# Kernel tuning notes

Measured on AMD Instinct MI355X. Metric: run time of the kernel, lower is better.

## Reference

```python
import jax, jax.numpy as jnp
import numpy as np

D_MODEL = 1024
N_HEADS = 16
D_HEAD = D_MODEL // N_HEADS
SCALE = 1.0 / np.sqrt(D_HEAD).astype(np.float32)


def _feature_map(x):
    # phi(x) = elu(x) + 1
    return jax.nn.elu(x) + 1.0


def setup_inputs() -> dict:
    key = jax.random.key(0)
    ks = jax.random.split(key, 7)
    b, s = 4, 2048
    w = 1.0 / np.sqrt(D_MODEL).astype(np.float32)
    return {
        "x": jax.random.normal(ks[0], (b, s, D_MODEL), dtype=jnp.float32),
        "Wq": jax.random.normal(ks[1], (D_MODEL, D_MODEL), dtype=jnp.float32) * w,
        "Wk": jax.random.normal(ks[2], (D_MODEL, D_MODEL), dtype=jnp.float32) * w,
        "Wv": jax.random.normal(ks[3], (D_MODEL, D_MODEL), dtype=jnp.float32) * w,
        "Wo": jax.random.normal(ks[4], (D_MODEL, D_MODEL), dtype=jnp.float32) * w,
        "Wg": jax.random.normal(ks[5], (N_HEADS, D_MODEL), dtype=jnp.float32) * w,
        "bg": jax.random.normal(ks[6], (N_HEADS,), dtype=jnp.float32) * 0.02,
    }


def reference(x, Wq, Wk, Wv, Wo, Wg, bg):
    b, s, _ = x.shape
    # projections (PyTorch Linear: y = x @ W.T)
    q = (x @ Wq.T).reshape(b, s, N_HEADS, D_HEAD)
    k = (x @ Wk.T).reshape(b, s, N_HEADS, D_HEAD)
    v = (x @ Wv.T).reshape(b, s, N_HEADS, D_HEAD)
    q = _feature_map(q * SCALE)
    k = _feature_map(k)
    gate = jax.nn.sigmoid(x @ Wg.T + bg)  # [b, s, h]

    # time-major for scan: [s, b, h, dh] and [s, b, h]
    qt = jnp.moveaxis(q, 1, 0)
    kt = jnp.moveaxis(k, 1, 0)
    vt = jnp.moveaxis(v, 1, 0)
    gt = jnp.moveaxis(gate, 1, 0)

    S0 = jnp.zeros((b, N_HEADS, D_HEAD, D_HEAD), dtype=x.dtype)

    def step(S, inp):
        q_t, k_t, v_t, g_t = inp
        # S_t = g_t * S_{t-1} + k_t v_t^T
        S = g_t[:, :, None, None] * S + k_t[..., :, None] * v_t[..., None, :]
        y_t = jnp.einsum("bhi,bhij->bhj", q_t, S)
        return S, y_t

    _, ys = jax.lax.scan(step, S0, (qt, kt, vt, gt))  # ys: [s, b, h, dh]
    y = jnp.moveaxis(ys, 0, 1).reshape(b, s, D_MODEL)
    return y @ Wo.T
```

## Files before the change

### kernel.cpp

```cpp
#include <hip/hip_runtime.h>
#include <hip/hip_bf16.h>
#include <math.h>

#define BATCH 4
#define SEQ 2048
#define DMODEL 1024
#define NHEADS 16
#define DHEAD 64
#define MTOK (BATCH * SEQ)
#define SCALE_Q 0.125f
#define NCHAIN (BATCH * NHEADS)
#define CT 64
#define NC (SEQ / CT)
#define SP 72
#define QKVS 3072
#define WROWS 4224

typedef unsigned short ushort_t;
typedef __attribute__((ext_vector_type(8))) short bf16x8;
typedef __attribute__((ext_vector_type(4))) float f32x4;

__device__ __forceinline__ float bf2f(unsigned short u) {
    return __uint_as_float(((unsigned)u) << 16);
}
__device__ __forceinline__ unsigned short f2bf(float f) {
    unsigned u = __float_as_uint(f);
    return (unsigned short)((u + 0x7fffu + ((u >> 16) & 1u)) >> 16);
}

__global__ __launch_bounds__(256) void cvt_all(const float* __restrict__ x,
                                               const float* __restrict__ Wq,
                                               const float* __restrict__ Wk,
                                               const float* __restrict__ Wv,
                                               const float* __restrict__ Wo,
                                               const float* __restrict__ Wg,
                                               ushort_t* __restrict__ xb,
                                               ushort_t* __restrict__ wcat) {
    const int blk = blockIdx.x;
    const int tid = threadIdx.x;

    if (blk < MTOK) {
        const float* xr = x + (size_t)blk * DMODEL;
        float4 v = ((const float4*)xr)[tid];
        ushort4 o;
        o.x = f2bf(v.x); o.y = f2bf(v.y); o.z = f2bf(v.z); o.w = f2bf(v.w);
        ((ushort4*)(xb + (size_t)blk * DMODEL))[tid] = o;
    } else {
        const int row = blk - MTOK;
        ushort4 o;
        if (row >= 3088 && row < 3200) {
            o.x = o.y = o.z = o.w = 0;
        } else {
            const float* src;
            if (row < 1024)      src = Wq + (size_t)row * DMODEL;
            else if (row < 2048) src = Wk + (size_t)(row - 1024) * DMODEL;
            else if (row < 3072) src = Wv + (size_t)(row - 2048) * DMODEL;
            else if (row < 3088) src = Wg + (size_t)(row - 3072) * DMODEL;
            else                 src = Wo + (size_t)(row - 3200) * DMODEL;
            float4 v = ((const float4*)src)[tid];
            o.x = f2bf(v.x); o.y = f2bf(v.y); o.z = f2bf(v.z); o.w = f2bf(v.w);
        }
        ((ushort4*)(wcat + (size_t)row * DMODEL))[tid] = o;
    }
}

#define GT 128
#define GBK 32

__global__ __launch_bounds__(256) void gemm_bf16(const ushort_t* __restrict__ A,
                                                 const ushort_t* __restrict__ B,
                                                 float* __restrict__ Cf,
                                                 ushort_t* __restrict__ Cb,
                                                 float* __restrict__ gatep,
                                                 const float* __restrict__ bgp,
                                                 int M, int N, int K,
                                                 int mode) {
    __shared__ ushort_t As[2][GT * GBK];
    __shared__ ushort_t Bs[2][GT * GBK];

    const int tid = threadIdx.x;
    const int w = tid >> 6;
    const int l = tid & 63;

    const int flat = blockIdx.x;
    const int kx = flat & 7;
    const int ii = flat >> 3;
    const int bx = ii >> 3;
    const int by = (kx << 3) | (ii & 7);
    const int m0 = by * GT;
    const int n0 = bx * GT;

    const int wm = (w >> 1) * 64;
    const int wn = (w & 1) * 64;

    const int srow = l >> 2;
    const int schunk = ((l & 3) ^ ((l >> 3) & 3)) * 8;

    const ushort_t* aseg[2];
    const ushort_t* bseg[2];
#pragma unroll
    for (int i = 0; i < 2; ++i) {
        const int s = w * 2 + i;
        aseg[i] = A + (size_t)(m0 + s * 16 + srow) * K + schunk;
        bseg[i] = B + (size_t)(n0 + s * 16 + srow) * K + schunk;
    }

#define STAGE(buf, k0)                                                          \
    do {                                                                        \
        _Pragma("unroll")                                                       \
        for (int i_ = 0; i_ < 2; ++i_) {                                        \
            const int s_ = w * 2 + i_;                                          \
            __builtin_amdgcn_global_load_lds(                                   \
                (const __attribute__((address_space(1))) unsigned int*)(const void*)(aseg[i_] + (k0)), \
                (__attribute__((address_space(3))) unsigned int*)(void*)&As[buf][s_ * 16 * GBK], \
                16, 0, 0);                                                      \
            __builtin_amdgcn_global_load_lds(                                   \
                (const __attribute__((address_space(1))) unsigned int*)(const void*)(bseg[i_] + (k0)), \
                (__attribute__((address_space(3))) unsigned int*)(void*)&Bs[buf][s_ * 16 * GBK], \
                16, 0, 0);                                                      \
        }                                                                       \
    } while (0)

    f32x4 acc[4][4];
#pragma unroll
    for (int i = 0; i < 4; ++i)
#pragma unroll
        for (int j = 0; j < 4; ++j)
#pragma unroll
            for (int r = 0; r < 4; ++r) acc[i][j][r] = 0.f;

    const int fr = l & 15;
    const int fsw = (((l >> 4) ^ ((fr >> 1) & 3))) * 8;

    STAGE(0, 0);

    const int nit = K / GBK;
    for (int it = 0; it < nit; ++it) {
        __syncthreads();
        if (it + 1 < nit) STAGE((it + 1) & 1, (it + 1) * GBK);

        const ushort_t* __restrict__ as = As[it & 1];
        const ushort_t* __restrict__ bs = Bs[it & 1];

        bf16x8 af[4], bfr[4];
#pragma unroll
        for (int ti = 0; ti < 4; ++ti)
            af[ti] = *(const bf16x8*)&as[(wm + ti * 16 + fr) * GBK + fsw];
#pragma unroll
        for (int tj = 0; tj < 4; ++tj)
            bfr[tj] = *(const bf16x8*)&bs[(wn + tj * 16 + fr) * GBK + fsw];
#pragma unroll
        for (int ti = 0; ti < 4; ++ti)
#pragma unroll
            for (int tj = 0; tj < 4; ++tj)
                acc[ti][tj] = __builtin_amdgcn_mfma_f32_16x16x32_bf16(
                    af[ti], bfr[tj], acc[ti][tj], 0, 0, 0);
    }
#undef STAGE

    const int er = (l >> 4) * 4;
    const int ec = l & 15;

    if (mode == 3 && n0 == 3072) {
#pragma unroll
        for (int ti = 0; ti < 4; ++ti)
#pragma unroll
            for (int r = 0; r < 4; ++r) {
                if (wn == 0) {
                    const int row = m0 + wm + ti * 16 + er + r;
                    const float vv = acc[ti][0][r] + bgp[ec];
                    gatep[(size_t)row * NHEADS + ec] = 1.f / (1.f + __expf(-vv));
                }
            }
        return;
    }

    float escale = 1.0f;
    bool do_phi = false;
    if (mode == 3) {
        do_phi = (n0 < 2048);
        escale = (n0 < 1024) ? SCALE_Q : 1.0f;
    }

#pragma unroll
    for (int ti = 0; ti < 4; ++ti)
#pragma unroll
        for (int tj = 0; tj < 4; ++tj)
#pragma unroll
            for (int r = 0; r < 4; ++r) {
                const int row = m0 + wm + ti * 16 + er + r;
                const int col = n0 + wn + tj * 16 + ec;
                float val = acc[ti][tj][r];
                if (mode == 0) {
                    Cf[(size_t)row * N + col] = val;
                } else {
                    val *= escale;
                    if (do_phi) val = (val > 0.f) ? (val + 1.f) : __expf(val);
                    Cb[(size_t)row * QKVS + col] = f2bf(val);
                }
            }
}

__global__ __launch_bounds__(256) void p1_kernel(const ushort_t* __restrict__ qkv,
                                                 const float* __restrict__ gate,
                                                 float* __restrict__ Dt,
                                                 float* __restrict__ Bg) {
    const int tile = blockIdx.x;
    const int chain = tile >> 5;
    const int c = tile & 31;
    const int b = chain >> 4;
    const int h = chain & 15;
    const int tid = threadIdx.x;
    const int w = tid >> 6;
    const int l = tid & 63;

    __shared__ ushort_t Kt[DHEAD * SP];
    __shared__ ushort_t Vt[DHEAD * SP];
    __shared__ float bs[CT];

    const int tau = tid >> 2;
    const int seg = (tid & 3) * 16;
    const size_t grow = ((size_t)(b * SEQ + c * CT + tau)) * QKVS + h * DHEAD + seg;
    union { float4 f4[2]; ushort_t us[16]; } uk, uv;
    uk.f4[0] = *(const float4*)&qkv[grow + 1024];
    uk.f4[1] = *(const float4*)&qkv[grow + 1024 + 8];
    uv.f4[0] = *(const float4*)&qkv[grow + 2048];
    uv.f4[1] = *(const float4*)&qkv[grow + 2048 + 8];

    if (tid < 64) {
        float g = gate[((size_t)(b * SEQ + c * CT + tid)) * NHEADS + h];
        float lg = __logf(g);
#pragma unroll
        for (int d = 1; d < 64; d <<= 1) {
            float n = __shfl_up(lg, d, 64);
            if (l >= d) lg += n;
        }
        bs[tid] = lg;
        if (tid == 63) Bg[tile] = lg;
    }
    __syncthreads();

    const float e = __expf(bs[63] - bs[tau]);
#pragma unroll
    for (int f = 0; f < 16; ++f) {
        Kt[(seg + f) * SP + tau] = f2bf(e * bf2f(uk.us[f]));
        Vt[(seg + f) * SP + tau] = uv.us[f];
    }
    __syncthreads();

    const int fr = l & 15;
    const int fq = (l >> 4) * 8;
    const int jw = w * 16;

    f32x4 accD[4];
#pragma unroll
    for (int nt = 0; nt < 4; ++nt)
#pragma unroll
        for (int r = 0; r < 4; ++r) accD[nt][r] = 0.f;

#pragma unroll
    for (int kc = 0; kc < 2; ++kc) {
        bf16x8 va = *(const bf16x8*)&Vt[(jw + fr) * SP + kc * 32 + fq];
#pragma unroll
        for (int nt = 0; nt < 4; ++nt) {
            bf16x8 kf = *(const bf16x8*)&Kt[(nt * 16 + fr) * SP + kc * 32 + fq];
            accD[nt] = __builtin_amdgcn_mfma_f32_16x16x32_bf16(va, kf, accD[nt], 0, 0, 0);
        }
    }

    const int er = (l >> 4) * 4;
    const size_t dbase = (size_t)tile * (DHEAD * DHEAD);
#pragma unroll
    for (int nt = 0; nt < 4; ++nt)
#pragma unroll
        for (int r = 0; r < 4; ++r) {
            const int j = jw + er + r;
            const int i = nt * 16 + fr;
            Dt[dbase + j * DHEAD + i] = accD[nt][r];
        }
}

__global__ __launch_bounds__(256) void p2_kernel(const float* __restrict__ Dt,
                                                 const float* __restrict__ Bg,
                                                 ushort_t* __restrict__ St) {
    const int chain = blockIdx.x >> 2;
    const int jq = (blockIdx.x & 3) * 16;
    const int tid = threadIdx.x;
    const int jj = jq + (tid >> 4);
    const int ii = (tid & 15) * 4;

    float4 S = make_float4(0.f, 0.f, 0.f, 0.f);
    for (int c = 0; c < NC; ++c) {
        const size_t base = (((size_t)chain * NC + c) * DHEAD + jj) * DHEAD + ii;
        ushort4 o;
        o.x = f2bf(S.x); o.y = f2bf(S.y); o.z = f2bf(S.z); o.w = f2bf(S.w);
        *(ushort4*)&St[base] = o;
        const float eB = __expf(Bg[chain * NC + c]);
        const float4 D = *(const float4*)&Dt[base];
        S.x = eB * S.x + D.x;
        S.y = eB * S.y + D.y;
        S.z = eB * S.z + D.z;
        S.w = eB * S.w + D.w;
    }
}

__global__ __launch_bounds__(256) void p3_kernel(const ushort_t* __restrict__ qkv,
                                                 const ushort_t* __restrict__ St,
                                                 const float* __restrict__ gate,
                                                 ushort_t* __restrict__ yb) {
    const int tile = blockIdx.x;
    const int chain = tile >> 5;
    const int c = tile & 31;
    const int b = chain >> 4;
    const int h = chain & 15;
    const int tid = threadIdx.x;
    const int w = tid >> 6;
    const int l = tid & 63;

    __shared__ ushort_t Qs[CT * SP];
    __shared__ ushort_t Ks[CT * SP];
    __shared__ ushort_t Vt[DHEAD * SP];
    __shared__ ushort_t Ss[CT * SP];
    __shared__ ushort_t Ps[CT * SP];
    __shared__ float bs[CT];

    {
        const int row = tid >> 2;
        const int seg = (tid & 3) * 16;
        const size_t grow = ((size_t)(b * SEQ + c * CT + row)) * QKVS + h * DHEAD + seg;
        float4 q0 = *(const float4*)&qkv[grow];
        float4 q1 = *(const float4*)&qkv[grow + 8];
        float4 k0 = *(const float4*)&qkv[grow + 1024];
        float4 k1 = *(const float4*)&qkv[grow + 1024 + 8];
        union { float4 f4[2]; ushort_t us[16]; } uv;
        uv.f4[0] = *(const float4*)&qkv[grow + 2048];
        uv.f4[1] = *(const float4*)&qkv[grow + 2048 + 8];
        const size_t srow = (((size_t)chain * NC + c) * DHEAD + row) * DHEAD + seg;
        float4 s0 = *(const float4*)&St[srow];
        float4 s1 = *(const float4*)&St[srow + 8];
        *(float4*)&Qs[row * SP + seg]     = q0;
        *(float4*)&Qs[row * SP + seg + 8] = q1;
        *(float4*)&Ks[row * SP + seg]     = k0;
        *(float4*)&Ks[row * SP + seg + 8] = k1;
        *(float4*)&Ss[row * SP + seg]     = s0;
        *(float4*)&Ss[row * SP + seg + 8] = s1;
#pragma unroll
        for (int f = 0; f < 16; ++f)
            Vt[(seg + f) * SP + row] = uv.us[f];
    }
    if (tid < 64) {
        float g = gate[((size_t)(b * SEQ + c * CT + tid)) * NHEADS + h];
        float lg = __logf(g);
#pragma unroll
        for (int d = 1; d < 64; d <<= 1) {
            float n = __shfl_up(lg, d, 64);
            if (l >= d) lg += n;
        }
        bs[tid] = lg;
    }
    __syncthreads();

    const int fr = l & 15;
    const int fq = (l >> 4) * 8;
    const int tw = w * 16;

    bf16x8 qa[2];
#pragma unroll
    for (int kc = 0; kc < 2; ++kc)
        qa[kc] = *(const bf16x8*)&Qs[(tw + fr) * SP + kc * 32 + fq];

    f32x4 accA[4], accP[4];
#pragma unroll
    for (int nt = 0; nt < 4; ++nt)
#pragma unroll
        for (int r = 0; r < 4; ++r) { accA[nt][r] = 0.f; accP[nt][r] = 0.f; }

#pragma unroll
    for (int kc = 0; kc < 2; ++kc)
#pragma unroll
        for (int nt = 0; nt < 4; ++nt) {
            bf16x8 sb = *(const bf16x8*)&Ss[(nt * 16 + fr) * SP + kc * 32 + fq];
            accA[nt] = __builtin_amdgcn_mfma_f32_16x16x32_bf16(qa[kc], sb, accA[nt], 0, 0, 0);
            bf16x8 kf = *(const bf16x8*)&Ks[(nt * 16 + fr) * SP + kc * 32 + fq];
            accP[nt] = __builtin_amdgcn_mfma_f32_16x16x32_bf16(qa[kc], kf, accP[nt], 0, 0, 0);
        }

    const int er = (l >> 4) * 4;
    int trow[4];
    float bt[4];
#pragma unroll
    for (int r = 0; r < 4; ++r) { trow[r] = tw + er + r; bt[r] = bs[trow[r]]; }
#pragma unroll
    for (int nt = 0; nt < 4; ++nt) {
        const int tau = nt * 16 + fr;
        const float btau = bs[tau];
#pragma unroll
        for (int r = 0; r < 4; ++r) {
            float f = (tau <= trow[r]) ? __expf(bt[r] - btau) : 0.f;
            Ps[trow[r] * SP + tau] = f2bf(accP[nt][r] * f);
        }
    }

    f32x4 accY[4];
#pragma unroll
    for (int r = 0; r < 4; ++r) {
        const float eb = __expf(bt[r]);
#pragma unroll
        for (int nt = 0; nt < 4; ++nt) accY[nt][r] = accA[nt][r] * eb;
    }
#pragma unroll
    for (int kc = 0; kc < 2; ++kc) {
        bf16x8 pa = *(const bf16x8*)&Ps[(tw + fr) * SP + kc * 32 + fq];
#pragma unroll
        for (int nt = 0; nt < 4; ++nt) {
            bf16x8 vf = *(const bf16x8*)&Vt[(nt * 16 + fr) * SP + kc * 32 + fq];
            accY[nt] = __builtin_amdgcn_mfma_f32_16x16x32_bf16(pa, vf, accY[nt], 0, 0, 0);
        }
    }

    const size_t ybase = ((size_t)(b * SEQ + c * CT)) * DMODEL + h * DHEAD;
#pragma unroll
    for (int nt = 0; nt < 4; ++nt)
#pragma unroll
        for (int r = 0; r < 4; ++r)
            yb[ybase + (size_t)trow[r] * DMODEL + nt * 16 + fr] = f2bf(accY[nt][r]);
}

extern "C" void kernel_launch(void* const* d_in, const int* in_sizes, int n_in,
                              void* d_out, int out_size, void* d_ws, size_t ws_size,
                              hipStream_t stream) {
    const float* x  = (const float*)d_in[0];
    const float* Wq = (const float*)d_in[1];
    const float* Wk = (const float*)d_in[2];
    const float* Wv = (const float*)d_in[3];
    const float* Wo = (const float*)d_in[4];
    const float* Wg = (const float*)d_in[5];
    const float* bg = (const float*)d_in[6];
    float* out = (float*)d_out;

    const size_t elems = (size_t)MTOK * DMODEL;
    const size_t welems = (size_t)DMODEL * DMODEL;
    const size_t stelems = (size_t)NCHAIN * NC * DHEAD * DHEAD;

    ushort_t* xb   = (ushort_t*)d_ws;
    ushort_t* St   = xb;
    ushort_t* qkv  = xb + elems;
    ushort_t* wcat = qkv + (size_t)MTOK * QKVS;
    float* gate    = (float*)(wcat + (size_t)WROWS * DMODEL);
    float* Bg      = gate + (size_t)MTOK * NHEADS;
    float* Dt      = Bg + (size_t)NCHAIN * NC;
    ushort_t* yb   = (ushort_t*)Dt;

    const size_t need = (size_t)((char*)(Dt + stelems) - (char*)d_ws);
    if (ws_size < need) return;

    cvt_all<<<dim3(MTOK + WROWS), dim3(256), 0, stream>>>(x, Wq, Wk, Wv, Wo, Wg, xb, wcat);

    gemm_bf16<<<dim3(25 * 64), dim3(256), 0, stream>>>(
        xb, wcat, nullptr, qkv, gate, bg, MTOK, QKVS, DMODEL, 3);

    p1_kernel<<<dim3(NCHAIN * NC), dim3(256), 0, stream>>>(qkv, gate, Dt, Bg);
    p2_kernel<<<dim3(NCHAIN * 4), dim3(256), 0, stream>>>(Dt, Bg, St);
    p3_kernel<<<dim3(NCHAIN * NC), dim3(256), 0, stream>>>(qkv, St, gate, yb);

    gemm_bf16<<<dim3(8 * 64), dim3(256), 0, stream>>>(
        yb, wcat + (size_t)3200 * DMODEL, out, nullptr, nullptr, nullptr,
        MTOK, DMODEL, DMODEL, 0);
}
```

Before: 243.2 us.

## Load GEMM B operand straight from global into registers, drop B LDS staging

```diff
diff --git a/kernel.cpp b/kernel.cpp
--- a/kernel.cpp
+++ b/kernel.cpp
@@ -76,20 +76,12 @@
                                                  int M, int N, int K,
                                                  int mode) {
     __shared__ ushort_t As[2][GT * GBK];
-    __shared__ ushort_t Bs[2][GT * GBK];
 
     const int tid = threadIdx.x;
     const int w = tid >> 6;
     const int l = tid & 63;
-
-    const int flat = blockIdx.x;
-    const int kx = flat & 7;
-    const int ii = flat >> 3;
-    const int bx = ii >> 3;
-    const int by = (kx << 3) | (ii & 7);
-    const int m0 = by * GT;
-    const int n0 = bx * GT;
-
+    const int m0 = blockIdx.y * GT;
+    const int n0 = blockIdx.x * GT;
     const int wm = (w >> 1) * 64;
     const int wn = (w & 1) * 64;
 
@@ -97,15 +89,13 @@
     const int schunk = ((l & 3) ^ ((l >> 3) & 3)) * 8;
 
     const ushort_t* aseg[2];
-    const ushort_t* bseg[2];
 #pragma unroll
     for (int i = 0; i < 2; ++i) {
         const int s = w * 2 + i;
         aseg[i] = A + (size_t)(m0 + s * 16 + srow) * K + schunk;
-        bseg[i] = B + (size_t)(n0 + s * 16 + srow) * K + schunk;
-    }
-
-#define STAGE(buf, k0)                                                          \
+    }
+
+#define STAGE_A(buf, k0)                                                        \
     do {                                                                        \
         _Pragma("unroll")                                                       \
         for (int i_ = 0; i_ < 2; ++i_) {                                        \
@@ -114,10 +104,6 @@
                 (const __attribute__((address_space(1))) unsigned int*)(const void*)(aseg[i_] + (k0)), \
                 (__attribute__((address_space(3))) unsigned int*)(void*)&As[buf][s_ * 16 * GBK], \
                 16, 0, 0);                                                      \
-            __builtin_amdgcn_global_load_lds(                                   \
-                (const __attribute__((address_space(1))) unsigned int*)(const void*)(bseg[i_] + (k0)), \
-                (__attribute__((address_space(3))) unsigned int*)(void*)&Bs[buf][s_ * 16 * GBK], \
-                16, 0, 0);                                                      \
         }                                                                       \
     } while (0)
 
@@ -130,33 +116,49 @@
             for (int r = 0; r < 4; ++r) acc[i][j][r] = 0.f;
 
     const int fr = l & 15;
+    const int fq = (l >> 4) * 8;
     const int fsw = (((l >> 4) ^ ((fr >> 1) & 3))) * 8;
 
-    STAGE(0, 0);
+    const ushort_t* bptr[4];
+#pragma unroll
+    for (int tj = 0; tj < 4; ++tj)
+        bptr[tj] = B + (size_t)(n0 + wn + tj * 16 + fr) * K + fq;
+
+    bf16x8 bcur[4], bnxt[4];
+
+    STAGE_A(0, 0);
+#pragma unroll
+    for (int tj = 0; tj < 4; ++tj)
+        bcur[tj] = *(const bf16x8*)(bptr[tj]);
 
     const int nit = K / GBK;
     for (int it = 0; it < nit; ++it) {
         __syncthreads();
-        if (it + 1 < nit) STAGE((it + 1) & 1, (it + 1) * GBK);
+        if (it + 1 < nit) {
+            STAGE_A((it + 1) & 1, (it + 1) * GBK);
+#pragma unroll
+            for (int tj = 0; tj < 4; ++tj)
+                bnxt[tj] = *(const bf16x8*)(bptr[tj] + (it + 1) * GBK);
+        }
 
         const ushort_t* __restrict__ as = As[it & 1];
-        const ushort_t* __restrict__ bs = Bs[it & 1];
-
-        bf16x8 af[4], bfr[4];
+        bf16x8 af[4];
 #pragma unroll
         for (int ti = 0; ti < 4; ++ti)
             af[ti] = *(const bf16x8*)&as[(wm + ti * 16 + fr) * GBK + fsw];
 #pragma unroll
-        for (int tj = 0; tj < 4; ++tj)
-            bfr[tj] = *(const bf16x8*)&bs[(wn + tj * 16 + fr) * GBK + fsw];
-#pragma unroll
         for (int ti = 0; ti < 4; ++ti)
 #pragma unroll
             for (int tj = 0; tj < 4; ++tj)
                 acc[ti][tj] = __builtin_amdgcn_mfma_f32_16x16x32_bf16(
-                    af[ti], bfr[tj], acc[ti][tj], 0, 0, 0);
-    }
-#undef STAGE
+                    af[ti], bcur[tj], acc[ti][tj], 0, 0, 0);
+
+        if (it + 1 < nit) {
+#pragma unroll
+            for (int tj = 0; tj < 4; ++tj) bcur[tj] = bnxt[tj];
+        }
+    }
+#undef STAGE_A
 
     const int er = (l >> 4) * 4;
     const int ec = l & 15;
@@ -439,7 +441,6 @@
     float* out = (float*)d_out;
 
     const size_t elems = (size_t)MTOK * DMODEL;
-    const size_t welems = (size_t)DMODEL * DMODEL;
     const size_t stelems = (size_t)NCHAIN * NC * DHEAD * DHEAD;
 
     ushort_t* xb   = (ushort_t*)d_ws;
@@ -456,14 +457,14 @@
 
     cvt_all<<<dim3(MTOK + WROWS), dim3(256), 0, stream>>>(x, Wq, Wk, Wv, Wo, Wg, xb, wcat);
 
-    gemm_bf16<<<dim3(25 * 64), dim3(256), 0, stream>>>(
+    gemm_bf16<<<dim3(25, MTOK / GT), dim3(256), 0, stream>>>(
         xb, wcat, nullptr, qkv, gate, bg, MTOK, QKVS, DMODEL, 3);
 
     p1_kernel<<<dim3(NCHAIN * NC), dim3(256), 0, stream>>>(qkv, gate, Dt, Bg);
     p2_kernel<<<dim3(NCHAIN * 4), dim3(256), 0, stream>>>(Dt, Bg, St);
     p3_kernel<<<dim3(NCHAIN * NC), dim3(256), 0, stream>>>(qkv, St, gate, yb);
 
-    gemm_bf16<<<dim3(8 * 64), dim3(256), 0, stream>>>(
+    gemm_bf16<<<dim3(DMODEL / GT, MTOK / GT), dim3(256), 0, stream>>>(
         yb, wcat + (size_t)3200 * DMODEL, out, nullptr, nullptr, nullptr,
         MTOK, DMODEL, DMODEL, 0);
 }
```

Result: slower. 313.7 us (+29.0%).
